# Kernel optimization log

Hardware: AMD Instinct MI355X
Metric: run time of the kernel (lower is better)

Reference implementation:

```python
import jax, jax.numpy as jnp
import numpy as np

N, E, B, L = 65536, 262144, 512, 1000
IN_DIM, HID, VOCAB = 74, 128, 25
CHANNELS = [HID, 96, 128, IN_DIM, HID]  # protein conv1d filter chain


def _conv1d(x, k):
    # x: [B, C_in, L], k: [C_out, C_in, 3], stride 1, padding 1 (like nn.Conv1d)
    return jax.lax.conv_general_dilated(x, k, (1,), ((1, 1),),
                                        dimension_numbers=('NCH', 'OIH', 'NCH'))


def setup_inputs() -> dict:
    key = jax.random.key(0)
    ks = jax.random.split(key, 20)

    def gl(k, shape, fan_in):
        return jax.random.normal(k, shape, jnp.float32) / np.float32(np.sqrt(fan_in))

    inp = {}
    inp['node_feats'] = jax.random.normal(ks[0], (N, IN_DIM), jnp.float32)
    # GraphConv (conv1): weight [in, hid]
    inp['W_gc'] = gl(ks[1], (IN_DIM, HID), IN_DIM)
    inp['b_gc'] = jnp.zeros((HID,), jnp.float32)
    # MLPNodeReadout: two linears (no activation between, per dgllife default)
    inp['W_ro_in'] = gl(ks[2], (HID, HID), HID)
    inp['b_ro_in'] = jnp.zeros((HID,), jnp.float32)
    inp['W_ro_out'] = gl(ks[3], (HID, HID), HID)
    inp['b_ro_out'] = jnp.zeros((HID,), jnp.float32)
    inp['Wc1'] = gl(ks[4], (HID, HID), HID); inp['bc1'] = jnp.zeros((HID,), jnp.float32)
    inp['Wc2'] = gl(ks[5], (HID, HID), HID); inp['bc2'] = jnp.zeros((HID,), jnp.float32)
    # protein embedding + 4 conv1d layers
    inp['embed'] = jax.random.normal(ks[6], (VOCAB, HID), jnp.float32)
    for i in range(4):
        cin, cout = CHANNELS[i], CHANNELS[i + 1]
        inp['K%d' % (i + 1)] = gl(ks[7 + i], (cout, cin, 3), cin * 3)
        inp['cb%d' % (i + 1)] = jnp.zeros((cout,), jnp.float32)
    # CPI head: Linear(2h,2h)+ReLU, Linear(2h,1)+Sigmoid
    inp['Wf1'] = gl(ks[11], (2 * HID, 2 * HID), 2 * HID); inp['bf1'] = jnp.zeros((2 * HID,), jnp.float32)
    inp['Wf2'] = gl(ks[12], (2 * HID, 1), 2 * HID); inp['bf2'] = jnp.zeros((1,), jnp.float32)
    # graph structure / protein tokens
    inp['edge_src'] = jax.random.randint(ks[13], (E,), 0, N, jnp.int32)
    inp['edge_dst'] = jax.random.randint(ks[14], (E,), 0, N, jnp.int32)
    inp['graph_ids'] = jnp.sort(jax.random.randint(ks[15], (N,), 0, B, jnp.int32))
    inp['protein_seq'] = jax.random.randint(ks[16], (B, L), 0, VOCAB, jnp.int32)
    return inp


def reference(node_feats, W_gc, b_gc, W_ro_in, b_ro_in, W_ro_out, b_ro_out,
              Wc1, bc1, Wc2, bc2, embed, K1, cb1, K2, cb2, K3, cb3, K4, cb4,
              Wf1, bf1, Wf2, bf2, edge_src, edge_dst, graph_ids, protein_seq):
    n = node_feats.shape[0]
    nb = protein_seq.shape[0]
    # dgl.add_self_loop: append self edges
    loop = jnp.arange(n, dtype=edge_src.dtype)
    src = jnp.concatenate([edge_src, loop])
    dst = jnp.concatenate([edge_dst, loop])
    ones = jnp.ones(src.shape[0], jnp.float32)
    deg_out = jax.ops.segment_sum(ones, src, n)  # out-degree (src norm)
    deg_in = jax.ops.segment_sum(ones, dst, n)   # in-degree (dst norm)
    h = node_feats * jax.lax.rsqrt(deg_out)[:, None]
    h = jax.ops.segment_sum(h[src], dst, n) * jax.lax.rsqrt(deg_in)[:, None]
    h = jax.nn.relu(h @ W_gc + b_gc)
    # MLPNodeReadout (sum over nodes per graph), then outer ReLU
    x = (h @ W_ro_in + b_ro_in) @ W_ro_out + b_ro_out
    hg = jax.nn.relu(jax.ops.segment_sum(x, graph_ids, nb))  # [B, HID]
    # compound FC layers (dropout = identity)
    cv = jax.nn.relu(hg @ Wc1 + bc1)
    cv = jax.nn.relu(cv @ Wc2 + bc2)
    pv = jnp.transpose(embed[protein_seq], (0, 2, 1))
    for K, b in ((K1, cb1), (K2, cb2), (K3, cb3), (K4, cb4)):
        pv = jax.nn.relu(_conv1d(pv, K) + b[None, :, None])
    pmax = jnp.max(pv, axis=-1)  # adaptive_max_pool1d(output_size=1) + squeeze
    # CPI head
    z = jnp.concatenate([cv, pmax], axis=1)  # [B, 2*HID]
    z = jax.nn.relu(z @ Wf1 + bf1)
    return jax.nn.sigmoid(z @ Wf2 + bf2)  # [B, 1]
```

## Files before the change

### kernel.cpp

```cpp
#include <hip/hip_runtime.h>
#include <math.h>

#define IN_DIM 74
#define HID 128
#define LSEQ 1000
#define RSA 272
#define RSB 208
#define TILE 48
#define R0 56
#define R1 54
#define R2 52
#define R3 50
#define NCHUNK 42
#define LDS_BIAS 24576
#define LDS_ACT  26368
#define ACTA_SZ  15232
#define ACTB_SZ  11232
#define ACTB_BASE (LDS_ACT + 2*ACTA_SZ)
#define LDS_TOTAL (ACTB_BASE + 2*ACTB_SZ)

typedef unsigned int u32;
typedef unsigned short u16;

typedef __attribute__((ext_vector_type(8))) short bf16x8;
typedef __attribute__((ext_vector_type(4))) float f32x4;

__device__ __forceinline__ u16 f2bf(float f){
  u32 u = __float_as_uint(f);
  u32 r = (u + 0x7fffu + ((u >> 16) & 1u)) >> 16;
  return (u16)r;
}
__device__ __forceinline__ u32 pack2(float x, float y){
  return (u32)f2bf(x) | ((u32)f2bf(y) << 16);
}

__global__ void k_cnt_edge(const int* __restrict__ src, const int* __restrict__ dst,
                           int* out_cnt, int* in_cnt, int E){
  int e = blockIdx.x*256 + threadIdx.x;
  if (e < E){ atomicAdd(&out_cnt[src[e]], 1); atomicAdd(&in_cnt[dst[e]], 1); }
}
__global__ void k_scan1(const int* __restrict__ cnt, int* pref, int* bsum, int N){
  __shared__ int buf[256];
  int t = threadIdx.x, i = blockIdx.x*256 + t;
  int v = (i < N) ? cnt[i] : 0;
  buf[t] = v; __syncthreads();
  for (int o = 1; o < 256; o <<= 1){
    int tv = (t >= o) ? buf[t-o] : 0;
    __syncthreads(); buf[t] += tv; __syncthreads();
  }
  if (i < N) pref[i] = buf[t] - v;
  if (t == 255) bsum[blockIdx.x] = buf[255];
}
__global__ void k_scan2(int* bsum, int nb){
  __shared__ int buf[1024];
  int t = threadIdx.x;
  int v = (t < nb) ? bsum[t] : 0;
  buf[t] = v; __syncthreads();
  for (int o = 1; o < 1024; o <<= 1){
    int tv = (t >= o) ? buf[t-o] : 0;
    __syncthreads(); buf[t] += tv; __syncthreads();
  }
  if (t < nb) bsum[t] = buf[t] - v;
}
__global__ void k_scan3(const int* __restrict__ pref, const int* __restrict__ bsum,
                        int* offs, int* cur, int N){
  int i = blockIdx.x*256 + threadIdx.x;
  if (i < N){ int o = pref[i] + bsum[blockIdx.x]; offs[i] = o; cur[i] = o; }
}
__global__ void k_csr_fill(const int* __restrict__ src, const int* __restrict__ dst,
                           int* cur, int* csr_src, int E){
  int e = blockIdx.x*256 + threadIdx.x;
  if (e < E){ int slot = atomicAdd(&cur[dst[e]], 1); csr_src[slot] = src[e]; }
}
__global__ __launch_bounds__(256) void k_gather(const float* __restrict__ nf,
    const int* __restrict__ csr_src, const int* __restrict__ offs,
    const int* __restrict__ in_cnt, const int* __restrict__ out_cnt,
    float* __restrict__ h_agg, int N){
  int wid = threadIdx.x >> 6, lane = threadIdx.x & 63;
  int d = blockIdx.x*4 + wid;
  if (d >= N) return;
  int beg = offs[d], num = in_cnt[d];
  const float* row = nf + (size_t)d*IN_DIM;
  float ws = rsqrtf((float)out_cnt[d] + 1.f);
  float a0 = row[lane]*ws, a1 = 0.f;
  if (lane < IN_DIM-64) a1 = row[64+lane]*ws;
  for (int j = 0; j < num; ++j){
    int s = csr_src[beg + j];
    float w = rsqrtf((float)out_cnt[s] + 1.f);
    const float* rs = nf + (size_t)s*IN_DIM;
    a0 += rs[lane]*w;
    if (lane < IN_DIM-64) a1 += rs[64+lane]*w;
  }
  float sc = rsqrtf((float)num + 1.f);
  float* hp = h_agg + (size_t)d*IN_DIM;
  hp[lane] = a0*sc;
  if (lane < IN_DIM-64) hp[64+lane] = a1*sc;
}
__global__ __launch_bounds__(256) void k_gc_gemm(const float* __restrict__ h_agg,
        const float* __restrict__ W, const float* __restrict__ bias,
        float* __restrict__ h, int N){
  __shared__ float Wl[IN_DIM*HID];
  __shared__ float rowsT[IN_DIM][36];
  int base = blockIdx.x * 32;
  for (int idx = threadIdx.x; idx < IN_DIM*HID; idx += 256) Wl[idx] = W[idx];
  for (int idx = threadIdx.x; idx < 32*IN_DIM; idx += 256){
    int r = idx / IN_DIM, k = idx - r*IN_DIM;
    rowsT[k][r] = (base + r < N) ? h_agg[(size_t)(base+r)*IN_DIM + k] : 0.f;
  }
  __syncthreads();
  int c = threadIdx.x & 127, rh = threadIdx.x >> 7;
  float acc[16];
  #pragma unroll
  for (int i = 0; i < 16; ++i) acc[i] = 0.f;
  for (int k = 0; k < IN_DIM; ++k){
    float w = Wl[k*HID + c];
    const float4* rp = (const float4*)&rowsT[k][rh*16];
    float4 r0 = rp[0], r1 = rp[1], r2 = rp[2], r3 = rp[3];
    acc[0] += r0.x*w; acc[1] += r0.y*w; acc[2] += r0.z*w; acc[3] += r0.w*w;
    acc[4] += r1.x*w; acc[5] += r1.y*w; acc[6] += r1.z*w; acc[7] += r1.w*w;
    acc[8] += r2.x*w; acc[9] += r2.y*w; acc[10] += r2.z*w; acc[11] += r2.w*w;
    acc[12] += r3.x*w; acc[13] += r3.y*w; acc[14] += r3.z*w; acc[15] += r3.w*w;
  }
  float bv = bias[c];
  #pragma unroll
  for (int i = 0; i < 16; ++i){
    int r = base + rh*16 + i;
    if (r < N) h[(size_t)r*HID + c] = fmaxf(acc[i] + bv, 0.f);
  }
}
__global__ __launch_bounds__(128) void k_graph_tail(const float* __restrict__ h,
    const int* __restrict__ gid,
    const float* __restrict__ W_ri, const float* __restrict__ b_ri,
    const float* __restrict__ W_ro, const float* __restrict__ b_ro,
    const float* __restrict__ Wc1, const float* __restrict__ bc1,
    const float* __restrict__ Wc2, const float* __restrict__ bc2,
    float* __restrict__ z, int N){
  __shared__ float va[128], vb[128];
  __shared__ int bounds[2];
  int g = blockIdx.x, c = threadIdx.x;
  if (c < 2){
    int target = g + c, lo = 0, hi = N;
    while (lo < hi){ int mid = (lo+hi)>>1; if (gid[mid] < target) lo = mid+1; else hi = mid; }
    bounds[c] = lo;
  }
  __syncthreads();
  int lo = bounds[0], hi = bounds[1];
  float s = 0.f;
  for (int i = lo; i < hi; ++i) s += h[(size_t)i*HID + c];
  va[c] = s;
  float cn = (float)(hi - lo);
  __syncthreads();
  s = 0.f;
  for (int k = 0; k < 128; ++k) s += va[k]*W_ri[k*128 + c];
  vb[c] = s + b_ri[c]*cn;
  __syncthreads();
  s = 0.f;
  for (int k = 0; k < 128; ++k) s += vb[k]*W_ro[k*128 + c];
  va[c] = fmaxf(s + b_ro[c]*cn, 0.f);
  __syncthreads();
  s = 0.f;
  for (int k = 0; k < 128; ++k) s += va[k]*Wc1[k*128 + c];
  vb[c] = fmaxf(s + bc1[c], 0.f);
  __syncthreads();
  s = 0.f;
  for (int k = 0; k < 128; ++k) s += vb[k]*Wc2[k*128 + c];
  z[(size_t)g*256 + c] = fmaxf(s + bc2[c], 0.f);
}

__global__ void k_setup(const float* __restrict__ K1, const float* __restrict__ K2,
                        const float* __restrict__ K3, const float* __restrict__ K4,
                        const float* __restrict__ cb1, const float* __restrict__ cb2,
                        const float* __restrict__ cb3, const float* __restrict__ cb4,
                        u16* __restrict__ AW, float* __restrict__ ball,
                        float* __restrict__ z, int* __restrict__ out_cnt,
                        int* __restrict__ in_cnt, int N, int B){
  int idx = blockIdx.x*256 + threadIdx.x;
  if (idx < NCHUNK*4096){
    int g = idx >> 12, rem = idx & 4095;
    int co = rem >> 5, kk = rem & 31;
    const float* Kw; int CIN, CPAD, COUT, ksl;
    if (g < 12)      { Kw = K1; CIN = 128; CPAD = 128; COUT =  96; ksl = g; }
    else if (g < 21) { Kw = K2; CIN =  96; CPAD =  96; COUT = 128; ksl = g-12; }
    else if (g < 33) { Kw = K3; CIN =  74; CPAD = 128; COUT =  74; ksl = g-21; }
    else             { Kw = K4; CIN =  74; CPAD =  96; COUT = 128; ksl = g-33; }
    int k = ksl*32 + kk;
    int t = k / CPAD, ci = k - t*CPAD;
    float v = (co < COUT && ci < CIN) ? Kw[((size_t)co*CIN + ci)*3 + t] : 0.f;
    int sl2 = (kk >> 3) ^ ((co >> 1) & 3);
    AW[(size_t)g*4096 + co*32 + sl2*8 + (kk & 7)] = f2bf(v);
    return;
  }
  idx -= NCHUNK*4096;
  if (idx < 448){
    float v = 0.f;
    if (idx < 96) v = cb1[idx];
    else if (idx < 224) v = cb2[idx-96];
    else if (idx < 320){ int c = idx-224; v = (c < 74) ? cb3[c] : 0.f; }
    else v = cb4[idx-320];
    ball[idx] = v;
    return;
  }
  idx -= 448;
  if (idx < B*128){ z[(size_t)(idx>>7)*256 + 128 + (idx&127)] = 0.f; return; }
  idx -= B*128;
  if (idx < 2*N){
    if (idx < N) out_cnt[idx] = 0; else in_cnt[idx-N] = 0;
  }
}

__device__ __forceinline__ void stage8k(char* lds, int tid, const u16* src, int pbuf){
  const char* s = (const char*)src;
  char* d = lds + pbuf*8192;
  __builtin_amdgcn_global_load_lds(
    (const __attribute__((address_space(1))) unsigned*)(s + tid*16),
    (__attribute__((address_space(3))) unsigned*)(d + tid*16), 16, 0, 0);
  __builtin_amdgcn_global_load_lds(
    (const __attribute__((address_space(1))) unsigned*)(s + 4096 + tid*16),
    (__attribute__((address_space(3))) unsigned*)(d + 4096 + tid*16), 16, 0, 0);
}

template<int KS, int G0, int M, int TPC, int RS_IN, int RCAP>
__device__ __forceinline__ void conv_phases(char* lds, const char* actIn,
    const u16* __restrict__ AW, int co0, int lm, int cg, int scg, int tid,
    f32x4 (&acc)[M][4])
{
  #pragma unroll
  for (int m = 0; m < M; ++m)
    #pragma unroll
    for (int n = 0; n < 4; ++n) acc[m][n] = (f32x4){0.f,0.f,0.f,0.f};
  #pragma unroll
  for (int ks = 0; ks < KS; ++ks){
    const int g = G0 + ks;
    if (g + 1 < NCHUNK) asm volatile("s_waitcnt vmcnt(2)");
    else                asm volatile("s_waitcnt vmcnt(0)");
    __builtin_amdgcn_s_barrier();
    __builtin_amdgcn_sched_barrier(0);
    if (g + 2 < NCHUNK) stage8k(lds, tid, AW + (size_t)(g+2)*4096, (g+2)%3);
    const char* wb = lds + (g%3)*8192;
    bf16x8 Af[M];
    #pragma unroll
    for (int m = 0; m < M; ++m)
      Af[m] = *(const bf16x8*)(wb + (co0 + m*16 + lm)*64 + scg*16);
    const int tap = ks / TPC;
    const int c16 = (ks - tap*TPC)*4 + cg;
    bf16x8 Bf[4];
    #pragma unroll
    for (int n = 0; n < 4; ++n){
      int raw = n*16 + lm + tap;
      int row = raw < RCAP ? raw : RCAP;
      Bf[n] = *(const bf16x8*)(actIn + row*RS_IN + c16*16);
    }
    __builtin_amdgcn_s_setprio(1);
    #pragma unroll
    for (int m = 0; m < M; ++m)
      #pragma unroll
      for (int n = 0; n < 4; ++n)
        acc[m][n] = __builtin_amdgcn_mfma_f32_16x16x32_bf16(Af[m], Bf[n], acc[m][n], 0, 0, 0);
    __builtin_amdgcn_s_setprio(0);
    asm volatile("s_waitcnt lgkmcnt(0)");
  }
}

template<int M>
__device__ __forceinline__ void epi_store(char* actOut, int RS_OUT,
    const float* lbias, int boff, int co0, int lm, int cg,
    int lbase, int nrows, f32x4 (&acc)[M][4])
{
  #pragma unroll
  for (int m = 0; m < M; ++m){
    int co = co0 + m*16 + cg*4;
    float4 bb = *(const float4*)(lbias + boff + co);
    #pragma unroll
    for (int n = 0; n < 4; ++n){
      int r1 = n*16 + lm;
      if (r1 < nrows){
        int l = lbase + r1;
        u32 lo = 0, hi = 0;
        if ((unsigned)l < (unsigned)LSEQ){
          f32x4 a = acc[m][n];
          lo = pack2(fmaxf(a[0]+bb.x, 0.f), fmaxf(a[1]+bb.y, 0.f));
          hi = pack2(fmaxf(a[2]+bb.z, 0.f), fmaxf(a[3]+bb.w, 0.f));
        }
        uint2 st; st.x = lo; st.y = hi;
        *(uint2*)(actOut + r1*RS_OUT + co*2) = st;
      }
    }
  }
  asm volatile("s_waitcnt lgkmcnt(0)");
}

__device__ __forceinline__ void epi_pool(const float* lbias, int boff,
    int co0, int lm, int cg, int l0, float* __restrict__ z, int b, f32x4 (&acc)[4][4])
{
  float mxv[4][4];
  #pragma unroll
  for (int m = 0; m < 4; ++m)
    #pragma unroll
    for (int j = 0; j < 4; ++j) mxv[m][j] = 0.f;
  #pragma unroll
  for (int m = 0; m < 4; ++m){
    float4 bb = *(const float4*)(lbias + boff + co0 + m*16 + cg*4);
    const float* bv = (const float*)&bb;
    #pragma unroll
    for (int n = 0; n < 4; ++n){
      int r1 = n*16 + lm;
      int l = l0 + r1;
      if (r1 < TILE && l < LSEQ){
        #pragma unroll
        for (int j = 0; j < 4; ++j)
          mxv[m][j] = fmaxf(mxv[m][j], fmaxf(acc[m][n][j] + bv[j], 0.f));
      }
    }
  }
  #pragma unroll
  for (int o = 1; o <= 8; o <<= 1)
    #pragma unroll
    for (int m = 0; m < 4; ++m)
      #pragma unroll
      for (int j = 0; j < 4; ++j)
        mxv[m][j] = fmaxf(mxv[m][j], __shfl_xor(mxv[m][j], o));
  if (lm == 0){
    float* zrow = z + (size_t)b*256 + 128;
    #pragma unroll
    for (int m = 0; m < 4; ++m)
      #pragma unroll
      for (int j = 0; j < 4; ++j)
        atomicMax((u32*)(zrow + co0 + m*16 + cg*4 + j), __float_as_uint(mxv[m][j]));
  }
}

__global__ __launch_bounds__(256, 2) void k_protein(
    const int* __restrict__ seq, const float* __restrict__ emb,
    const u16* __restrict__ AW, const float* __restrict__ ball,
    float* __restrict__ z)
{
  __shared__ __align__(16) char lds[LDS_TOTAL];
  const int tid = threadIdx.x;
  const int lane = tid & 63, wid = tid >> 6;
  const int lm = lane & 15, cg = lane >> 4;
  const int scg = cg ^ ((lm >> 1) & 3);
  const int tl = wid >> 1;
  const int h  = wid & 1;
  const int b  = blockIdx.y;
  const int l0 = (blockIdx.x*2 + tl) * TILE;

  for (int i = tid; i < 448; i += 256) ((float*)(lds + LDS_BIAS))[i] = ball[i];

  for (int idx = tid; idx < 2*R0*16; idx += 256){
    int t2 = idx / (R0*16), rem = idx - t2*(R0*16);
    int r = rem >> 4, p = rem & 15;
    int ll0 = (blockIdx.x*2 + t2) * TILE;
    int l = ll0 - 4 + r;
    uint4 st = make_uint4(0u,0u,0u,0u);
    if ((unsigned)l < (unsigned)LSEQ){
      int tok = seq[b*LSEQ + l];
      const float4* e = (const float4*)(emb + (size_t)tok*HID + p*8);
      float4 v0 = e[0], v1 = e[1];
      st.x = pack2(v0.x, v0.y); st.y = pack2(v0.z, v0.w);
      st.z = pack2(v1.x, v1.y); st.w = pack2(v1.z, v1.w);
    }
    *(uint4*)(lds + LDS_ACT + t2*ACTA_SZ + r*RSA + p*16) = st;
  }
  asm volatile("s_waitcnt vmcnt(0)");
  stage8k(lds, tid, AW, 0);
  stage8k(lds, tid, AW + 4096, 1);
  asm volatile("s_waitcnt lgkmcnt(0)");

  char* actA = lds + LDS_ACT + tl*ACTA_SZ;
  char* actB = lds + ACTB_BASE + tl*ACTB_SZ;
  const float* lbias = (const float*)(lds + LDS_BIAS);

  {
    f32x4 acc[3][4];
    conv_phases<12,0,3,4,RSA,R0-1>(lds, actA, AW, h*48, lm, cg, scg, tid, acc);
    epi_store<3>(actB, RSB, lbias, 0, h*48, lm, cg, l0-3, R1, acc);
  }
  {
    f32x4 acc[4][4];
    conv_phases<9,12,4,3,RSB,R1-1>(lds, actB, AW, h*64, lm, cg, scg, tid, acc);
    epi_store<4>(actA, RSA, lbias, 96, h*64, lm, cg, l0-2, R2, acc);
  }
  {
    f32x4 acc[3][4];
    conv_phases<12,21,3,4,RSA,R2-1>(lds, actA, AW, h*48, lm, cg, scg, tid, acc);
    epi_store<3>(actB, RSB, lbias, 224, h*48, lm, cg, l0-1, R3, acc);
  }
  {
    f32x4 acc[4][4];
    conv_phases<9,33,4,3,RSB,R3-1>(lds, actB, AW, h*64, lm, cg, scg, tid, acc);
    epi_pool(lbias, 320, h*64, lm, cg, l0, z, b, acc);
  }
}

__global__ __launch_bounds__(256) void k_fc_head(const float* __restrict__ z,
    const float* __restrict__ Wf1, const float* __restrict__ bf1,
    const float* __restrict__ Wf2, const float* __restrict__ bf2v,
    float* __restrict__ out){
  __shared__ float za[256];
  __shared__ float red[4];
  int r = blockIdx.x, c = threadIdx.x;
  za[c] = z[(size_t)r*256 + c];
  __syncthreads();
  float s = 0.f;
  for (int k = 0; k < 256; ++k) s += za[k]*Wf1[(size_t)k*256 + c];
  s = fmaxf(s + bf1[c], 0.f);
  float p = s * Wf2[c];
  for (int o = 32; o; o >>= 1) p += __shfl_xor(p, o);
  if ((c & 63) == 0) red[c >> 6] = p;
  __syncthreads();
  if (c == 0) out[r] = 1.f/(1.f + __expf(-(red[0]+red[1]+red[2]+red[3] + bf2v[0])));
}

extern "C" void kernel_launch(void* const* d_in, const int* in_sizes, int n_in,
                              void* d_out, int out_size, void* d_ws, size_t ws_size,
                              hipStream_t stream){
  const float* nf   = (const float*)d_in[0];
  const float* W_gc = (const float*)d_in[1];
  const float* b_gc = (const float*)d_in[2];
  const float* W_ri = (const float*)d_in[3];
  const float* b_ri = (const float*)d_in[4];
  const float* W_ro = (const float*)d_in[5];
  const float* b_ro = (const float*)d_in[6];
  const float* Wc1  = (const float*)d_in[7];
  const float* bc1  = (const float*)d_in[8];
  const float* Wc2  = (const float*)d_in[9];
  const float* bc2  = (const float*)d_in[10];
  const float* emb  = (const float*)d_in[11];
  const float* K1 = (const float*)d_in[12]; const float* cb1 = (const float*)d_in[13];
  const float* K2 = (const float*)d_in[14]; const float* cb2 = (const float*)d_in[15];
  const float* K3 = (const float*)d_in[16]; const float* cb3 = (const float*)d_in[17];
  const float* K4 = (const float*)d_in[18]; const float* cb4 = (const float*)d_in[19];
  const float* Wf1 = (const float*)d_in[20]; const float* bf1 = (const float*)d_in[21];
  const float* Wf2 = (const float*)d_in[22]; const float* bf2v = (const float*)d_in[23];
  const int* esrc = (const int*)d_in[24];
  const int* edst = (const int*)d_in[25];
  const int* gids = (const int*)d_in[26];
  const int* seq  = (const int*)d_in[27];
  float* out = (float*)d_out;

  int N = in_sizes[26];
  int E = in_sizes[24];
  int B = out_size;
  int nb = (N + 255)/256;

  char* ws = (char*)d_ws;
  size_t off = 0;
  auto take = [&](size_t bytes)->char*{
    char* p = ws + off; off = (off + bytes + 255) & ~(size_t)255; return p;
  };
  float* z      = (float*)take((size_t)B*2*HID*4);
  int* out_cnt  = (int*)take((size_t)N*4);
  int* in_cnt   = (int*)take((size_t)N*4);
  int* pref     = (int*)take((size_t)N*4);
  int* offs     = (int*)take((size_t)N*4);
  int* cur      = (int*)take((size_t)N*4);
  int* bsum     = (int*)take(1024*4);
  int* csr_src  = (int*)take((size_t)E*4);
  u16* AW       = (u16*)take((size_t)NCHUNK*8192);
  float* ball   = (float*)take(448*4);
  float* h_agg  = (float*)take((size_t)N*IN_DIM*4);
  float* h      = (float*)take((size_t)N*HID*4);

  int setup_total = NCHUNK*4096 + 448 + B*128 + 2*N;
  k_setup<<<(setup_total+255)/256, 256, 0, stream>>>(K1, K2, K3, K4, cb1, cb2, cb3, cb4,
                                                     AW, ball, z, out_cnt, in_cnt, N, B);

  k_cnt_edge<<<(E+255)/256, 256, 0, stream>>>(esrc, edst, out_cnt, in_cnt, E);
  k_scan1<<<nb, 256, 0, stream>>>(in_cnt, pref, bsum, N);
  k_scan2<<<1, 1024, 0, stream>>>(bsum, nb);
  k_scan3<<<nb, 256, 0, stream>>>(pref, bsum, offs, cur, N);
  k_csr_fill<<<(E+255)/256, 256, 0, stream>>>(esrc, edst, cur, csr_src, E);
  k_gather<<<(N+3)/4, 256, 0, stream>>>(nf, csr_src, offs, in_cnt, out_cnt, h_agg, N);
  k_gc_gemm<<<(N+31)/32, 256, 0, stream>>>(h_agg, W_gc, b_gc, h, N);
  k_graph_tail<<<B, 128, 0, stream>>>(h, gids, W_ri, b_ri, W_ro, b_ro,
                                      Wc1, bc1, Wc2, bc2, z, N);

  dim3 pgrid(11, B);
  k_protein<<<pgrid, 256, 0, stream>>>(seq, emb, AW, ball, z);

  k_fc_head<<<B, 256, 0, stream>>>(z, Wf1, bf1, Wf2, bf2v, out);
}
```

Before: 435.7 us.

## Widen protein conv blocks to four tiles and stage weights in 24KB groups

The fused protein conv kernel now runs 512-thread blocks covering four sequence tiles of 50 positions, where it used to run two tiles of 48. Weights are double-buffered in 24KB groups of three chunks, so the per-chunk barrier and async stage become one sync every three chunks. Larger blocks share each weight load across more tiles, which cuts global weight traffic and barrier count. The cost is one block per CU, a larger LDS footprint, less latency hiding between blocks, and more complex prefetch bookkeeping across layer boundaries.

```diff
diff --git a/kernel.cpp b/kernel.cpp
--- a/kernel.cpp
+++ b/kernel.cpp
@@ -6,18 +6,20 @@
 #define LSEQ 1000
 #define RSA 272
 #define RSB 208
-#define TILE 48
-#define R0 56
-#define R1 54
-#define R2 52
-#define R3 50
+#define TILE 50
+#define R0 58
+#define R1 56
+#define R2 54
+#define R3 52
 #define NCHUNK 42
-#define LDS_BIAS 24576
-#define LDS_ACT  26368
-#define ACTA_SZ  15232
-#define ACTB_SZ  11232
-#define ACTB_BASE (LDS_ACT + 2*ACTA_SZ)
-#define LDS_TOTAL (ACTB_BASE + 2*ACTB_SZ)
+#define NGRP 14
+#define WBUF_SZ 24576
+#define LDS_BIAS 49152
+#define LDS_ACT  50944
+#define ACTA_SZ  15776
+#define ACTB_SZ  11648
+#define ACTB_BASE (LDS_ACT + 4*ACTA_SZ)
+#define LDS_TOTAL (ACTB_BASE + 4*ACTB_SZ)
 
 typedef unsigned int u32;
 typedef unsigned short u16;
@@ -208,15 +210,14 @@
   }
 }
 
-__device__ __forceinline__ void stage8k(char* lds, int tid, const u16* src, int pbuf){
+__device__ __forceinline__ void stage24k(char* lds, int tid, const u16* src, int pbuf){
   const char* s = (const char*)src;
-  char* d = lds + pbuf*8192;
-  __builtin_amdgcn_global_load_lds(
-    (const __attribute__((address_space(1))) unsigned*)(s + tid*16),
-    (__attribute__((address_space(3))) unsigned*)(d + tid*16), 16, 0, 0);
-  __builtin_amdgcn_global_load_lds(
-    (const __attribute__((address_space(1))) unsigned*)(s + 4096 + tid*16),
-    (__attribute__((address_space(3))) unsigned*)(d + 4096 + tid*16), 16, 0, 0);
+  char* d = lds + pbuf*WBUF_SZ;
+  #pragma unroll
+  for (int i = 0; i < 3; ++i)
+    __builtin_amdgcn_global_load_lds(
+      (const __attribute__((address_space(1))) unsigned*)(s + i*8192 + tid*16),
+      (__attribute__((address_space(3))) unsigned*)(d + i*8192 + tid*16), 16, 0, 0);
 }
 
 template<int KS, int G0, int M, int TPC, int RS_IN, int RCAP>
@@ -231,12 +232,7 @@
   #pragma unroll
   for (int ks = 0; ks < KS; ++ks){
     const int g = G0 + ks;
-    if (g + 1 < NCHUNK) asm volatile("s_waitcnt vmcnt(2)");
-    else                asm volatile("s_waitcnt vmcnt(0)");
-    __builtin_amdgcn_s_barrier();
-    __builtin_amdgcn_sched_barrier(0);
-    if (g + 2 < NCHUNK) stage8k(lds, tid, AW + (size_t)(g+2)*4096, (g+2)%3);
-    const char* wb = lds + (g%3)*8192;
+    const char* wb = lds + ((g/3)&1)*WBUF_SZ + (g%3)*8192;
     bf16x8 Af[M];
     #pragma unroll
     for (int m = 0; m < M; ++m)
@@ -257,7 +253,11 @@
       for (int n = 0; n < 4; ++n)
         acc[m][n] = __builtin_amdgcn_mfma_f32_16x16x32_bf16(Af[m], Bf[n], acc[m][n], 0, 0, 0);
     __builtin_amdgcn_s_setprio(0);
-    asm volatile("s_waitcnt lgkmcnt(0)");
+    if ((g % 3) == 2 && (ks + 1 < KS)){
+      __syncthreads();
+      const int gn = g/3 + 2;
+      if (gn < NGRP) stage24k(lds, tid, AW + (size_t)gn*12288, gn & 1);
+    }
   }
 }
 
@@ -286,7 +286,6 @@
       }
     }
   }
-  asm volatile("s_waitcnt lgkmcnt(0)");
 }
 
 __device__ __forceinline__ void epi_pool(const float* lbias, int boff,
@@ -329,7 +328,7 @@
   }
 }
 
-__global__ __launch_bounds__(256, 2) void k_protein(
+__global__ __launch_bounds__(512, 1) void k_protein(
     const int* __restrict__ seq, const float* __restrict__ emb,
     const u16* __restrict__ AW, const float* __restrict__ ball,
     float* __restrict__ z)
@@ -342,14 +341,14 @@
   const int tl = wid >> 1;
   const int h  = wid & 1;
   const int b  = blockIdx.y;
-  const int l0 = (blockIdx.x*2 + tl) * TILE;
-
-  for (int i = tid; i < 448; i += 256) ((float*)(lds + LDS_BIAS))[i] = ball[i];
-
-  for (int idx = tid; idx < 2*R0*16; idx += 256){
+  const int l0 = (blockIdx.x*4 + tl) * TILE;
+
+  for (int i = tid; i < 448; i += 512) ((float*)(lds + LDS_BIAS))[i] = ball[i];
+
+  for (int idx = tid; idx < 4*R0*16; idx += 512){
     int t2 = idx / (R0*16), rem = idx - t2*(R0*16);
     int r = rem >> 4, p = rem & 15;
-    int ll0 = (blockIdx.x*2 + t2) * TILE;
+    int ll0 = (blockIdx.x*4 + t2) * TILE;
     int l = ll0 - 4 + r;
     uint4 st = make_uint4(0u,0u,0u,0u);
     if ((unsigned)l < (unsigned)LSEQ){
@@ -361,10 +360,9 @@
     }
     *(uint4*)(lds + LDS_ACT + t2*ACTA_SZ + r*RSA + p*16) = st;
   }
-  asm volatile("s_waitcnt vmcnt(0)");
-  stage8k(lds, tid, AW, 0);
-  stage8k(lds, tid, AW + 4096, 1);
-  asm volatile("s_waitcnt lgkmcnt(0)");
+  stage24k(lds, tid, AW, 0);
+  stage24k(lds, tid, AW + 12288, 1);
+  __syncthreads();
 
   char* actA = lds + LDS_ACT + tl*ACTA_SZ;
   char* actB = lds + ACTB_BASE + tl*ACTB_SZ;
@@ -374,16 +372,22 @@
     f32x4 acc[3][4];
     conv_phases<12,0,3,4,RSA,R0-1>(lds, actA, AW, h*48, lm, cg, scg, tid, acc);
     epi_store<3>(actB, RSB, lbias, 0, h*48, lm, cg, l0-3, R1, acc);
+    __syncthreads();
+    stage24k(lds, tid, AW + (size_t)5*12288, 5 & 1);
   }
   {
     f32x4 acc[4][4];
     conv_phases<9,12,4,3,RSB,R1-1>(lds, actB, AW, h*64, lm, cg, scg, tid, acc);
     epi_store<4>(actA, RSA, lbias, 96, h*64, lm, cg, l0-2, R2, acc);
+    __syncthreads();
+    stage24k(lds, tid, AW + (size_t)8*12288, 8 & 1);
   }
   {
     f32x4 acc[3][4];
     conv_phases<12,21,3,4,RSA,R2-1>(lds, actA, AW, h*48, lm, cg, scg, tid, acc);
     epi_store<3>(actB, RSB, lbias, 224, h*48, lm, cg, l0-1, R3, acc);
+    __syncthreads();
+    stage24k(lds, tid, AW + (size_t)12*12288, 12 & 1);
   }
   {
     f32x4 acc[4][4];
@@ -475,8 +479,8 @@
   k_graph_tail<<<B, 128, 0, stream>>>(h, gids, W_ri, b_ri, W_ro, b_ro,
                                       Wc1, bc1, Wc2, bc2, z, N);
 
-  dim3 pgrid(11, B);
-  k_protein<<<pgrid, 256, 0, stream>>>(seq, emb, AW, ball, z);
+  dim3 pgrid(5, B);
+  k_protein<<<pgrid, 512, 0, stream>>>(seq, emb, AW, ball, z);
 
   k_fc_head<<<B, 256, 0, stream>>>(z, Wf1, bf1, Wf2, bf2v, out);
 }
```

Result: faster. 423.4 us (-2.8%).
